# Kernel optimization log

Hardware: AMD Instinct MI355X
Metric: run time of the kernel (lower is better)

Reference implementation:

```python
import jax, jax.numpy as jnp
import numpy as np

B, C, L, K = 8, 128, 32768, 129  # batch, seq_len (channels), samples, filter length


def setup_inputs() -> dict:
    key = jax.random.key(0)
    k0, k1, k2, k3 = jax.random.split(key, 4)
    return {
        "x": jax.random.normal(k0, (B, C, L), dtype=jnp.float32),
        "weights_mag": jnp.ones((C, 1), dtype=jnp.float32),
        "weights_angle": jax.random.uniform(k1, (C, 1), dtype=jnp.float32),
        "kernel_real": jax.random.normal(k2, (K,), dtype=jnp.float32),
        "kernel_imag": jax.random.normal(k3, (K,), dtype=jnp.float32),
    }


def _matched_filter(x, kr, ki):
    # PyTorch F.conv1d is cross-correlation; mf_coeffs = conj(kernel) repeated per
    # channel (groups = C), so every channel is correlated with the SAME conj kernel.
    # Input is real (x.to(complex64) has zero imag), so:
    #   out = corr(x, conj(k)) = corr(x, kr) - 1j * corr(x, ki)
    b, c, l = x.shape
    kk = kr.shape[0]
    pad = kk // 2
    w = jnp.stack([kr, -ki])[:, None, :]  # [2, 1, K]: real and imag of conj kernel
    y = jax.lax.conv_general_dilated(
        x.reshape(b * c, 1, l), w,
        window_strides=(1,), padding=[(pad, pad)],
        dimension_numbers=("NCH", "OIH", "NCH"),
    )  # [B*C, 2, L]
    yr = y[:, 0].reshape(b, c, l)
    yi = y[:, 1].reshape(b, c, l)
    return yr + 1j * yi  # complex64


def reference(x, weights_mag, weights_angle, kernel_real, kernel_imag):
    batch = x.shape[0]
    y = _matched_filter(x, kernel_real, kernel_imag)          # [B, C, L] complex64
    phase = jnp.arctan(weights_angle)                          # [C, 1]
    norm_mag = batch * jax.nn.softmax(weights_mag, axis=0)     # [C, 1]
    scale = (norm_mag.astype(jnp.complex64) * jnp.exp(-1j * phase))  # [C, 1] complex
    return scale * y
```

## Files before the change

### kernel.cpp

```cpp
#include <hip/hip_runtime.h>
#include <hip/hip_bf16.h>
#include <math.h>

constexpr int Bc = 8, Cc = 128, Lc = 32768, Kc = 129, PAD = Kc / 2;

constexpr int ROWS   = 16;
constexpr int MLEN   = 1024;
constexpr int PSPAN  = MLEN + 144;
constexpr int PSTR   = 1176;
constexpr int THREADS= 256;
constexpr int NTILES = MLEN / 16;
constexpr int NWAVES = THREADS / 64;
constexpr int TPW    = NTILES / NWAVES;
constexpr int NQ     = PSPAN / 4;
constexpr int NF     = 19;

typedef __attribute__((ext_vector_type(8))) short short8;
typedef __attribute__((ext_vector_type(4))) float floatx4;

__device__ __forceinline__ unsigned short f2bf(float f) {
    return __builtin_bit_cast(unsigned short, __float2bfloat16(f));
}

__global__ void scale_kernel(const float* __restrict__ wm,
                             const float* __restrict__ wa,
                             float* __restrict__ ws, int C, float batchf) {
    int c = threadIdx.x;
    if (c >= C) return;
    float m = -1e30f;
    for (int i = 0; i < C; ++i) m = fmaxf(m, wm[i]);
    float s = 0.f;
    for (int i = 0; i < C; ++i) s += expf(wm[i] - m);
    float nm = batchf * expf(wm[c] - m) / s;
    float a = wa[c];
    float inv = rsqrtf(1.f + a * a);
    ws[2 * c]     = nm * inv;
    ws[2 * c + 1] = nm * a * inv;
}

__global__ __launch_bounds__(THREADS, 4)
void mf_kernel(const float* __restrict__ x,
               const float* __restrict__ kr,
               const float* __restrict__ ki,
               const float* __restrict__ sc_ss,
               float* __restrict__ out, int interleaved) {
    __shared__ __align__(16) unsigned short lx[ROWS * PSTR];

    const int bx   = blockIdx.x;
    const int bg   = blockIdx.y;
    const int row0 = bg * ROWS;
    const int P0   = bx * MLEN;
    const int s0   = P0 - PAD;

    const int tid  = threadIdx.x;
    const int lane = tid & 63;
    const int fh   = lane >> 4;
    const int fn   = lane & 15;
    const int wv   = tid >> 6;

    short8 ar[5], ai[5];
    #pragma unroll
    for (int d = 0; d < 5; ++d) {
        #pragma unroll
        for (int e = 0; e < 8; ++e) {
            int idx = 32 * d + 8 * fh + e - fn;
            bool ok = (idx >= 0) && (idx < Kc);
            ar[d][e] = (short)f2bf(ok ? kr[idx] : 0.f);
            ai[d][e] = (short)f2bf(ok ? ki[idx] : 0.f);
        }
    }

    const int srow = tid >> 4;
    const int scol = tid & 15;
    const float* __restrict__ xr = x + (size_t)(row0 + srow) * Lc;
    unsigned short* lrow = &lx[srow * PSTR];
    const bool interior = (s0 >= 0) && (s0 + PSPAN <= Lc);
    #pragma unroll
    for (int i = 0; i < NF; ++i) {
        const int i4 = scol + 16 * i;
        if (i4 < NQ) {
            const int g = s0 + 4 * i4;
            float4 v;
            if (interior) {
                v = *reinterpret_cast<const float4*>(xr + g);
            } else {
                v.x = (g + 0 >= 0 && g + 0 < Lc) ? xr[g + 0] : 0.f;
                v.y = (g + 1 >= 0 && g + 1 < Lc) ? xr[g + 1] : 0.f;
                v.z = (g + 2 >= 0 && g + 2 < Lc) ? xr[g + 2] : 0.f;
                v.w = (g + 3 >= 0 && g + 3 < Lc) ? xr[g + 3] : 0.f;
            }
            __hip_bfloat162 p0 = __float22bfloat162_rn(make_float2(v.x, v.y));
            __hip_bfloat162 p1 = __float22bfloat162_rn(make_float2(v.z, v.w));
            ushort2 u0, u1;
            __builtin_memcpy(&u0, &p0, 4);
            __builtin_memcpy(&u1, &p1, 4);
            ushort4 h;
            h.x = u0.x; h.y = u0.y; h.z = u1.x; h.w = u1.y;
            *reinterpret_cast<ushort4*>(&lrow[4 * i4]) = h;
        }
    }
    __syncthreads();

    const int ch = (row0 + fn) & (Cc - 1);
    const float scv = sc_ss[2 * ch];
    const float ssv = sc_ss[2 * ch + 1];

    #pragma unroll
    for (int jj = 0; jj < TPW; ++jj) {
        const int j  = wv * TPW + jj;
        const int pb = 16 * j;
        const unsigned short* lp = &lx[fn * PSTR + pb + 8 * fh];
        floatx4 cr = {0.f, 0.f, 0.f, 0.f};
        floatx4 cim = {0.f, 0.f, 0.f, 0.f};
        #pragma unroll
        for (int d = 0; d < 5; ++d) {
            short8 b = *reinterpret_cast<const short8*>(lp + 32 * d);
            cr  = __builtin_amdgcn_mfma_f32_16x16x32_bf16(ar[d], b, cr, 0, 0, 0);
            cim = __builtin_amdgcn_mfma_f32_16x16x32_bf16(ai[d], b, cim, 0, 0, 0);
        }
        const size_t obase = (size_t)(row0 + fn) * Lc + P0 + pb + 4 * fh;
        if (!interleaved) {
            float4 o;
            o.x = scv * cr[0] - ssv * cim[0];
            o.y = scv * cr[1] - ssv * cim[1];
            o.z = scv * cr[2] - ssv * cim[2];
            o.w = scv * cr[3] - ssv * cim[3];
            *reinterpret_cast<float4*>(out + obase) = o;
        } else {
            float2* o2 = reinterpret_cast<float2*>(out) + obase;
            #pragma unroll
            for (int r = 0; r < 4; ++r) {
                o2[r] = make_float2(scv * cr[r] - ssv * cim[r],
                                    -scv * cim[r] - ssv * cr[r]);
            }
        }
    }
}

extern "C" void kernel_launch(void* const* d_in, const int* in_sizes, int n_in,
                              void* d_out, int out_size, void* d_ws, size_t ws_size,
                              hipStream_t stream) {
    const float* x  = (const float*)d_in[0];
    const float* wm = (const float*)d_in[1];
    const float* wa = (const float*)d_in[2];
    const float* kr = (const float*)d_in[3];
    const float* ki = (const float*)d_in[4];
    float* out = (float*)d_out;
    float* ws  = (float*)d_ws;

    const int C = in_sizes[1];
    const long long N = (long long)Bc * Cc * Lc;
    const int interleaved = (out_size == 2 * N) ? 1 : 0;

    hipLaunchKernelGGL(scale_kernel, dim3(1), dim3(C), 0, stream,
                       wm, wa, ws, C, (float)Bc);

    dim3 grid(Lc / MLEN, (Bc * Cc) / ROWS);
    hipLaunchKernelGGL(mf_kernel, grid, dim3(THREADS), 0, stream,
                       x, kr, ki, ws, out, interleaved);
}
```

Before: 78.77 us.

## Batch global loads ahead of filter build and swizzle block order across L

Interior blocks now issue the first ten float4 global loads up front, build the bf16 filter fragments while those loads are in flight, then convert and store them and issue the remaining loads in a second batch. This is meant to hide global-load latency behind the kernel-fragment setup and keep more memory requests outstanding. The block x index is also permuted so consecutively scheduled blocks touch spread-out L segments, which may change cache and channel locality. The cost is higher register pressure from holding up to ten float4 values at once, which could hurt occupancy under the launch bound of four blocks.

New measurement: 112.7 us. 1.43x slower.

```diff
diff --git a/kernel.cpp b/kernel.cpp
--- a/kernel.cpp
+++ b/kernel.cpp
@@ -14,6 +14,8 @@
 constexpr int TPW    = NTILES / NWAVES;
 constexpr int NQ     = PSPAN / 4;
 constexpr int NF     = 19;
+constexpr int NB1    = 10;
+constexpr int NB2    = NF - NB1;
 
 typedef __attribute__((ext_vector_type(8))) short short8;
 typedef __attribute__((ext_vector_type(4))) float floatx4;
@@ -46,7 +48,7 @@
                float* __restrict__ out, int interleaved) {
     __shared__ __align__(16) unsigned short lx[ROWS * PSTR];
 
-    const int bx   = blockIdx.x;
+    const int bx   = ((blockIdx.x & 7) << 2) | (blockIdx.x >> 3);
     const int bg   = blockIdx.y;
     const int row0 = bg * ROWS;
     const int P0   = bx * MLEN;
@@ -58,45 +60,72 @@
     const int fn   = lane & 15;
     const int wv   = tid >> 6;
 
-    short8 ar[5], ai[5];
-    #pragma unroll
-    for (int d = 0; d < 5; ++d) {
-        #pragma unroll
-        for (int e = 0; e < 8; ++e) {
-            int idx = 32 * d + 8 * fh + e - fn;
-            bool ok = (idx >= 0) && (idx < Kc);
-            ar[d][e] = (short)f2bf(ok ? kr[idx] : 0.f);
-            ai[d][e] = (short)f2bf(ok ? ki[idx] : 0.f);
-        }
-    }
-
     const int srow = tid >> 4;
     const int scol = tid & 15;
     const float* __restrict__ xr = x + (size_t)(row0 + srow) * Lc;
     unsigned short* lrow = &lx[srow * PSTR];
     const bool interior = (s0 >= 0) && (s0 + PSPAN <= Lc);
-    #pragma unroll
-    for (int i = 0; i < NF; ++i) {
-        const int i4 = scol + 16 * i;
-        if (i4 < NQ) {
-            const int g = s0 + 4 * i4;
-            float4 v;
-            if (interior) {
-                v = *reinterpret_cast<const float4*>(xr + g);
-            } else {
+
+    short8 ar[5], ai[5];
+
+    auto BUILD_A = [&]() {
+        #pragma unroll
+        for (int d = 0; d < 5; ++d) {
+            #pragma unroll
+            for (int e = 0; e < 8; ++e) {
+                int idx = 32 * d + 8 * fh + e - fn;
+                bool ok = (idx >= 0) && (idx < Kc);
+                ar[d][e] = (short)f2bf(ok ? kr[idx] : 0.f);
+                ai[d][e] = (short)f2bf(ok ? ki[idx] : 0.f);
+            }
+        }
+    };
+
+    auto CVTW = [&](int i4, const float4& v) {
+        __hip_bfloat162 p0 = __float22bfloat162_rn(make_float2(v.x, v.y));
+        __hip_bfloat162 p1 = __float22bfloat162_rn(make_float2(v.z, v.w));
+        ushort2 u0, u1;
+        __builtin_memcpy(&u0, &p0, 4);
+        __builtin_memcpy(&u1, &p1, 4);
+        ushort4 h;
+        h.x = u0.x; h.y = u0.y; h.z = u1.x; h.w = u1.y;
+        *reinterpret_cast<ushort4*>(&lrow[4 * i4]) = h;
+    };
+
+    if (interior) {
+        float4 va[NB1];
+        #pragma unroll
+        for (int i = 0; i < NB1; ++i) {
+            va[i] = *reinterpret_cast<const float4*>(xr + s0 + 4 * (scol + 16 * i));
+        }
+        BUILD_A();
+        #pragma unroll
+        for (int i = 0; i < NB1; ++i) CVTW(scol + 16 * i, va[i]);
+        float4 vb[NB2];
+        #pragma unroll
+        for (int i = 0; i < NB2; ++i) {
+            const int i4 = scol + 16 * (NB1 + i);
+            if (i4 < NQ) vb[i] = *reinterpret_cast<const float4*>(xr + s0 + 4 * i4);
+        }
+        #pragma unroll
+        for (int i = 0; i < NB2; ++i) {
+            const int i4 = scol + 16 * (NB1 + i);
+            if (i4 < NQ) CVTW(i4, vb[i]);
+        }
+    } else {
+        BUILD_A();
+        #pragma unroll
+        for (int i = 0; i < NF; ++i) {
+            const int i4 = scol + 16 * i;
+            if (i4 < NQ) {
+                const int g = s0 + 4 * i4;
+                float4 v;
                 v.x = (g + 0 >= 0 && g + 0 < Lc) ? xr[g + 0] : 0.f;
                 v.y = (g + 1 >= 0 && g + 1 < Lc) ? xr[g + 1] : 0.f;
                 v.z = (g + 2 >= 0 && g + 2 < Lc) ? xr[g + 2] : 0.f;
                 v.w = (g + 3 >= 0 && g + 3 < Lc) ? xr[g + 3] : 0.f;
+                CVTW(i4, v);
             }
-            __hip_bfloat162 p0 = __float22bfloat162_rn(make_float2(v.x, v.y));
-            __hip_bfloat162 p1 = __float22bfloat162_rn(make_float2(v.z, v.w));
-            ushort2 u0, u1;
-            __builtin_memcpy(&u0, &p0, 4);
-            __builtin_memcpy(&u1, &p1, 4);
-            ushort4 h;
-            h.x = u0.x; h.y = u0.y; h.z = u1.x; h.w = u1.y;
-            *reinterpret_cast<ushort4*>(&lrow[4 * i4]) = h;
         }
     }
     __syncthreads();
```

## Load input directly from global into MFMA operands, dropping LDS staging

Applied to the files above, without the earlier changes.

Removes the shared-memory staging of the bf16 input tile and the block barrier. Each lane now reads its MFMA B operand straight from global memory per output tile and converts it to bf16 in registers. This saves LDS traffic and the sync, but each input element is now fetched several times across overlapping windows and relies on L1/L2 to absorb the reuse. Occupancy hint raised from 4 to 5 blocks per SM.

After: 199.8 us. 2.54x slower.

```diff
diff --git a/kernel.cpp b/kernel.cpp
--- a/kernel.cpp
+++ b/kernel.cpp
@@ -6,20 +6,32 @@
 
 constexpr int ROWS   = 16;
 constexpr int MLEN   = 1024;
-constexpr int PSPAN  = MLEN + 144;
-constexpr int PSTR   = 1176;
 constexpr int THREADS= 256;
-constexpr int NTILES = MLEN / 16;
-constexpr int NWAVES = THREADS / 64;
-constexpr int TPW    = NTILES / NWAVES;
-constexpr int NQ     = PSPAN / 4;
-constexpr int NF     = 19;
+constexpr int TPW    = 16;
 
 typedef __attribute__((ext_vector_type(8))) short short8;
 typedef __attribute__((ext_vector_type(4))) float floatx4;
 
 __device__ __forceinline__ unsigned short f2bf(float f) {
     return __builtin_bit_cast(unsigned short, __float2bfloat16(f));
+}
+
+__device__ __forceinline__ short8 cvt8(const float4& a, const float4& b) {
+    __hip_bfloat162 p0 = __float22bfloat162_rn(make_float2(a.x, a.y));
+    __hip_bfloat162 p1 = __float22bfloat162_rn(make_float2(a.z, a.w));
+    __hip_bfloat162 p2 = __float22bfloat162_rn(make_float2(b.x, b.y));
+    __hip_bfloat162 p3 = __float22bfloat162_rn(make_float2(b.z, b.w));
+    ushort2 u0, u1, u2, u3;
+    __builtin_memcpy(&u0, &p0, 4);
+    __builtin_memcpy(&u1, &p1, 4);
+    __builtin_memcpy(&u2, &p2, 4);
+    __builtin_memcpy(&u3, &p3, 4);
+    short8 r;
+    r[0] = (short)u0.x; r[1] = (short)u0.y;
+    r[2] = (short)u1.x; r[3] = (short)u1.y;
+    r[4] = (short)u2.x; r[5] = (short)u2.y;
+    r[6] = (short)u3.x; r[7] = (short)u3.y;
+    return r;
 }
 
 __global__ void scale_kernel(const float* __restrict__ wm,
@@ -38,19 +50,16 @@
     ws[2 * c + 1] = nm * a * inv;
 }
 
-__global__ __launch_bounds__(THREADS, 4)
+__global__ __launch_bounds__(THREADS, 5)
 void mf_kernel(const float* __restrict__ x,
                const float* __restrict__ kr,
                const float* __restrict__ ki,
                const float* __restrict__ sc_ss,
                float* __restrict__ out, int interleaved) {
-    __shared__ __align__(16) unsigned short lx[ROWS * PSTR];
-
     const int bx   = blockIdx.x;
     const int bg   = blockIdx.y;
     const int row0 = bg * ROWS;
     const int P0   = bx * MLEN;
-    const int s0   = P0 - PAD;
 
     const int tid  = threadIdx.x;
     const int lane = tid & 63;
@@ -70,55 +79,54 @@
         }
     }
 
-    const int srow = tid >> 4;
-    const int scol = tid & 15;
-    const float* __restrict__ xr = x + (size_t)(row0 + srow) * Lc;
-    unsigned short* lrow = &lx[srow * PSTR];
-    const bool interior = (s0 >= 0) && (s0 + PSPAN <= Lc);
-    #pragma unroll
-    for (int i = 0; i < NF; ++i) {
-        const int i4 = scol + 16 * i;
-        if (i4 < NQ) {
-            const int g = s0 + 4 * i4;
-            float4 v;
-            if (interior) {
-                v = *reinterpret_cast<const float4*>(xr + g);
-            } else {
-                v.x = (g + 0 >= 0 && g + 0 < Lc) ? xr[g + 0] : 0.f;
-                v.y = (g + 1 >= 0 && g + 1 < Lc) ? xr[g + 1] : 0.f;
-                v.z = (g + 2 >= 0 && g + 2 < Lc) ? xr[g + 2] : 0.f;
-                v.w = (g + 3 >= 0 && g + 3 < Lc) ? xr[g + 3] : 0.f;
-            }
-            __hip_bfloat162 p0 = __float22bfloat162_rn(make_float2(v.x, v.y));
-            __hip_bfloat162 p1 = __float22bfloat162_rn(make_float2(v.z, v.w));
-            ushort2 u0, u1;
-            __builtin_memcpy(&u0, &p0, 4);
-            __builtin_memcpy(&u1, &p1, 4);
-            ushort4 h;
-            h.x = u0.x; h.y = u0.y; h.z = u1.x; h.w = u1.y;
-            *reinterpret_cast<ushort4*>(&lrow[4 * i4]) = h;
-        }
-    }
-    __syncthreads();
-
     const int ch = (row0 + fn) & (Cc - 1);
     const float scv = sc_ss[2 * ch];
     const float ssv = sc_ss[2 * ch + 1];
 
+    const float* __restrict__ xrow = x + (size_t)(row0 + fn) * Lc;
+    const int j0 = (P0 >> 4) + wv * TPW;
+    const float* p = xrow + (16 * j0 - PAD + 8 * fh);
+
     #pragma unroll
-    for (int jj = 0; jj < TPW; ++jj) {
-        const int j  = wv * TPW + jj;
-        const int pb = 16 * j;
-        const unsigned short* lp = &lx[fn * PSTR + pb + 8 * fh];
-        floatx4 cr = {0.f, 0.f, 0.f, 0.f};
+    for (int jj = 0; jj < TPW; ++jj, p += 16) {
+        const int jt = j0 + jj;
+        const int sb = 16 * jt - PAD;
+        floatx4 cr  = {0.f, 0.f, 0.f, 0.f};
         floatx4 cim = {0.f, 0.f, 0.f, 0.f};
-        #pragma unroll
-        for (int d = 0; d < 5; ++d) {
-            short8 b = *reinterpret_cast<const short8*>(lp + 32 * d);
-            cr  = __builtin_amdgcn_mfma_f32_16x16x32_bf16(ar[d], b, cr, 0, 0, 0);
-            cim = __builtin_amdgcn_mfma_f32_16x16x32_bf16(ai[d], b, cim, 0, 0, 0);
+
+        if (sb >= 0 && sb + 160 <= Lc) {
+            float4 f[10];
+            #pragma unroll
+            for (int d = 0; d < 5; ++d) {
+                f[2 * d]     = *reinterpret_cast<const float4*>(p + 32 * d);
+                f[2 * d + 1] = *reinterpret_cast<const float4*>(p + 32 * d + 4);
+            }
+            #pragma unroll
+            for (int d = 0; d < 5; ++d) {
+                short8 b = cvt8(f[2 * d], f[2 * d + 1]);
+                cr  = __builtin_amdgcn_mfma_f32_16x16x32_bf16(ar[d], b, cr, 0, 0, 0);
+                cim = __builtin_amdgcn_mfma_f32_16x16x32_bf16(ai[d], b, cim, 0, 0, 0);
+            }
+        } else {
+            #pragma unroll
+            for (int d = 0; d < 5; ++d) {
+                float4 va, vb;
+                const int g0 = sb + 32 * d + 8 * fh;
+                va.x = (g0 + 0 >= 0 && g0 + 0 < Lc) ? xrow[g0 + 0] : 0.f;
+                va.y = (g0 + 1 >= 0 && g0 + 1 < Lc) ? xrow[g0 + 1] : 0.f;
+                va.z = (g0 + 2 >= 0 && g0 + 2 < Lc) ? xrow[g0 + 2] : 0.f;
+                va.w = (g0 + 3 >= 0 && g0 + 3 < Lc) ? xrow[g0 + 3] : 0.f;
+                vb.x = (g0 + 4 >= 0 && g0 + 4 < Lc) ? xrow[g0 + 4] : 0.f;
+                vb.y = (g0 + 5 >= 0 && g0 + 5 < Lc) ? xrow[g0 + 5] : 0.f;
+                vb.z = (g0 + 6 >= 0 && g0 + 6 < Lc) ? xrow[g0 + 6] : 0.f;
+                vb.w = (g0 + 7 >= 0 && g0 + 7 < Lc) ? xrow[g0 + 7] : 0.f;
+                short8 b = cvt8(va, vb);
+                cr  = __builtin_amdgcn_mfma_f32_16x16x32_bf16(ar[d], b, cr, 0, 0, 0);
+                cim = __builtin_amdgcn_mfma_f32_16x16x32_bf16(ai[d], b, cim, 0, 0, 0);
+            }
         }
-        const size_t obase = (size_t)(row0 + fn) * Lc + P0 + pb + 4 * fh;
+
+        const size_t obase = (size_t)(row0 + fn) * Lc + 16 * jt + 4 * fh;
         if (!interleaved) {
             float4 o;
             o.x = scv * cr[0] - ssv * cim[0];
```

## Pipeline input staging with async global-to-LDS loads over multiple chunks per block

Applied to the files above, without the earlier changes.

Each block now handles four consecutive 512-sample chunks with 512 threads. The next chunk's fp32 input is fetched straight into LDS with global_load_lds while MFMAs run on the current chunk, then converted to bf16 in a separate LDS buffer. The intent is to hide global load latency and spread the kernel-coefficient setup across more work. The cost is extra LDS traffic for the fp32 staging copy, more barriers per chunk, fewer blocks in the grid, and a halo of 256 samples loaded per 512 outputs rather than 144 per 1024.

New measurement: 77.66 us. No clear change (-1.4%).

```diff
diff --git a/kernel.cpp b/kernel.cpp
--- a/kernel.cpp
+++ b/kernel.cpp
@@ -5,21 +5,25 @@
 constexpr int Bc = 8, Cc = 128, Lc = 32768, Kc = 129, PAD = Kc / 2;
 
 constexpr int ROWS   = 16;
-constexpr int MLEN   = 1024;
-constexpr int PSPAN  = MLEN + 144;
-constexpr int PSTR   = 1176;
-constexpr int THREADS= 256;
-constexpr int NTILES = MLEN / 16;
-constexpr int NWAVES = THREADS / 64;
-constexpr int TPW    = NTILES / NWAVES;
-constexpr int NQ     = PSPAN / 4;
-constexpr int NF     = 19;
+constexpr int MLEN   = 512;
+constexpr int NCH    = 4;
+constexpr int STG    = 768;
+constexpr int F32STR = 772;
+constexpr int BF_STR = 776;
+constexpr int THREADS= 512;
+constexpr int TPW    = 4;
 
 typedef __attribute__((ext_vector_type(8))) short short8;
 typedef __attribute__((ext_vector_type(4))) float floatx4;
 
 __device__ __forceinline__ unsigned short f2bf(float f) {
     return __builtin_bit_cast(unsigned short, __float2bfloat16(f));
+}
+
+__device__ __forceinline__ void gload_lds16(const float* g, void* l) {
+    auto gp = (const __attribute__((address_space(1))) void*)g;
+    auto lp = (__attribute__((address_space(3))) void*)l;
+    __builtin_amdgcn_global_load_lds(gp, lp, 16, 0, 0);
 }
 
 __global__ void scale_kernel(const float* __restrict__ wm,
@@ -44,19 +48,18 @@
                const float* __restrict__ ki,
                const float* __restrict__ sc_ss,
                float* __restrict__ out, int interleaved) {
-    __shared__ __align__(16) unsigned short lx[ROWS * PSTR];
+    __shared__ __align__(16) float          lf[ROWS * F32STR];
+    __shared__ __align__(16) unsigned short lb[ROWS * BF_STR];
 
     const int bx   = blockIdx.x;
     const int bg   = blockIdx.y;
     const int row0 = bg * ROWS;
-    const int P0   = bx * MLEN;
-    const int s0   = P0 - PAD;
 
     const int tid  = threadIdx.x;
     const int lane = tid & 63;
+    const int wv   = tid >> 6;
     const int fh   = lane >> 4;
     const int fn   = lane & 15;
-    const int wv   = tid >> 6;
 
     short8 ar[5], ai[5];
     #pragma unroll
@@ -69,71 +72,116 @@
             ai[d][e] = (short)f2bf(ok ? ki[idx] : 0.f);
         }
     }
-
-    const int srow = tid >> 4;
-    const int scol = tid & 15;
-    const float* __restrict__ xr = x + (size_t)(row0 + srow) * Lc;
-    unsigned short* lrow = &lx[srow * PSTR];
-    const bool interior = (s0 >= 0) && (s0 + PSPAN <= Lc);
-    #pragma unroll
-    for (int i = 0; i < NF; ++i) {
-        const int i4 = scol + 16 * i;
-        if (i4 < NQ) {
-            const int g = s0 + 4 * i4;
-            float4 v;
-            if (interior) {
-                v = *reinterpret_cast<const float4*>(xr + g);
-            } else {
-                v.x = (g + 0 >= 0 && g + 0 < Lc) ? xr[g + 0] : 0.f;
-                v.y = (g + 1 >= 0 && g + 1 < Lc) ? xr[g + 1] : 0.f;
-                v.z = (g + 2 >= 0 && g + 2 < Lc) ? xr[g + 2] : 0.f;
-                v.w = (g + 3 >= 0 && g + 3 < Lc) ? xr[g + 3] : 0.f;
-            }
-            __hip_bfloat162 p0 = __float22bfloat162_rn(make_float2(v.x, v.y));
-            __hip_bfloat162 p1 = __float22bfloat162_rn(make_float2(v.z, v.w));
-            ushort2 u0, u1;
-            __builtin_memcpy(&u0, &p0, 4);
-            __builtin_memcpy(&u1, &p1, 4);
-            ushort4 h;
-            h.x = u0.x; h.y = u0.y; h.z = u1.x; h.w = u1.y;
-            *reinterpret_cast<ushort4*>(&lrow[4 * i4]) = h;
-        }
-    }
-    __syncthreads();
-
     const int ch = (row0 + fn) & (Cc - 1);
     const float scv = sc_ss[2 * ch];
     const float ssv = sc_ss[2 * ch + 1];
 
-    #pragma unroll
-    for (int jj = 0; jj < TPW; ++jj) {
-        const int j  = wv * TPW + jj;
-        const int pb = 16 * j;
-        const unsigned short* lp = &lx[fn * PSTR + pb + 8 * fh];
-        floatx4 cr = {0.f, 0.f, 0.f, 0.f};
-        floatx4 cim = {0.f, 0.f, 0.f, 0.f};
-        #pragma unroll
-        for (int d = 0; d < 5; ++d) {
-            short8 b = *reinterpret_cast<const short8*>(lp + 32 * d);
-            cr  = __builtin_amdgcn_mfma_f32_16x16x32_bf16(ar[d], b, cr, 0, 0, 0);
-            cim = __builtin_amdgcn_mfma_f32_16x16x32_bf16(ai[d], b, cim, 0, 0, 0);
-        }
-        const size_t obase = (size_t)(row0 + fn) * Lc + P0 + pb + 4 * fh;
-        if (!interleaved) {
-            float4 o;
-            o.x = scv * cr[0] - ssv * cim[0];
-            o.y = scv * cr[1] - ssv * cim[1];
-            o.z = scv * cr[2] - ssv * cim[2];
-            o.w = scv * cr[3] - ssv * cim[3];
-            *reinterpret_cast<float4*>(out + obase) = o;
+    auto s0_of = [&](int c) { return (bx * NCH + c) * MLEN - 2 * PAD + 64; };
+
+    auto is_edge = [&](int c) {
+        const int s0 = (bx * NCH + c) * MLEN - 64;
+        return (s0 < 0) || (s0 + STG > Lc);
+    };
+
+    auto DMA_STAGE = [&](int c) {
+        const int s0 = (bx * NCH + c) * MLEN - 64;
+        #pragma unroll
+        for (int rr = 0; rr < 2; ++rr) {
+            const int r = 2 * wv + rr;
+            const float* xr = x + (size_t)(row0 + r) * Lc + s0 + 4 * lane;
+            #pragma unroll
+            for (int p = 0; p < 3; ++p) {
+                gload_lds16(xr + 256 * p, (char*)lf + 3088 * r + 1024 * p);
+            }
+        }
+    };
+
+    auto EDGE_STAGE = [&](int c) {
+        const int s0 = (bx * NCH + c) * MLEN - 64;
+        const int r = tid >> 5;
+        const int scol = tid & 31;
+        const float* xr = x + (size_t)(row0 + r) * Lc;
+        #pragma unroll
+        for (int i = 0; i < 6; ++i) {
+            const int c4 = 4 * (scol + 32 * i);
+            const int g = s0 + c4;
+            float4 v;
+            v.x = (g + 0 >= 0 && g + 0 < Lc) ? xr[g + 0] : 0.f;
+            v.y = (g + 1 >= 0 && g + 1 < Lc) ? xr[g + 1] : 0.f;
+            v.z = (g + 2 >= 0 && g + 2 < Lc) ? xr[g + 2] : 0.f;
+            v.w = (g + 3 >= 0 && g + 3 < Lc) ? xr[g + 3] : 0.f;
+            *reinterpret_cast<float4*>(&lf[F32STR * r + c4]) = v;
+        }
+    };
+
+    auto CONV = [&]() {
+        #pragma unroll
+        for (int rr = 0; rr < 2; ++rr) {
+            const int r = 2 * wv + rr;
+            #pragma unroll
+            for (int p = 0; p < 3; ++p) {
+                const int dw = 256 * p + 4 * lane;
+                float4 v = *reinterpret_cast<const float4*>(&lf[F32STR * r + dw]);
+                __hip_bfloat162 p0 = __float22bfloat162_rn(make_float2(v.x, v.y));
+                __hip_bfloat162 p1 = __float22bfloat162_rn(make_float2(v.z, v.w));
+                ushort2 u0, u1;
+                __builtin_memcpy(&u0, &p0, 4);
+                __builtin_memcpy(&u1, &p1, 4);
+                ushort4 h; h.x = u0.x; h.y = u0.y; h.z = u1.x; h.w = u1.y;
+                *reinterpret_cast<ushort4*>(&lb[BF_STR * r + dw]) = h;
+            }
+        }
+    };
+
+    auto COMPUTE = [&](int c) {
+        const int P0 = (bx * NCH + c) * MLEN;
+        #pragma unroll
+        for (int jj = 0; jj < TPW; ++jj) {
+            const int j = wv * TPW + jj;
+            floatx4 cr = {0.f, 0.f, 0.f, 0.f};
+            floatx4 cim = {0.f, 0.f, 0.f, 0.f};
+            const unsigned short* lp = &lb[BF_STR * fn + 16 * j + 8 * fh];
+            #pragma unroll
+            for (int d = 0; d < 5; ++d) {
+                short8 b = *reinterpret_cast<const short8*>(lp + 32 * d);
+                cr  = __builtin_amdgcn_mfma_f32_16x16x32_bf16(ar[d], b, cr, 0, 0, 0);
+                cim = __builtin_amdgcn_mfma_f32_16x16x32_bf16(ai[d], b, cim, 0, 0, 0);
+            }
+            const size_t obase = (size_t)(row0 + fn) * Lc + P0 + 16 * j + 4 * fh;
+            if (!interleaved) {
+                float4 o;
+                o.x = scv * cr[0] - ssv * cim[0];
+                o.y = scv * cr[1] - ssv * cim[1];
+                o.z = scv * cr[2] - ssv * cim[2];
+                o.w = scv * cr[3] - ssv * cim[3];
+                *reinterpret_cast<float4*>(out + obase) = o;
+            } else {
+                float2* o2 = reinterpret_cast<float2*>(out) + obase;
+                #pragma unroll
+                for (int r = 0; r < 4; ++r) {
+                    o2[r] = make_float2(scv * cr[r] - ssv * cim[r],
+                                        -scv * cim[r] - ssv * cr[r]);
+                }
+            }
+        }
+    };
+
+    if (!is_edge(0)) DMA_STAGE(0);
+
+    #pragma unroll 1
+    for (int c = 0; c < NCH; ++c) {
+        if (is_edge(c)) {
+            EDGE_STAGE(c);
+            __syncthreads();
         } else {
-            float2* o2 = reinterpret_cast<float2*>(out) + obase;
-            #pragma unroll
-            for (int r = 0; r < 4; ++r) {
-                o2[r] = make_float2(scv * cr[r] - ssv * cim[r],
-                                    -scv * cim[r] - ssv * cr[r]);
-            }
-        }
+            asm volatile("s_waitcnt vmcnt(0)" ::: "memory");
+            __builtin_amdgcn_sched_barrier(0);
+        }
+        CONV();
+        __syncthreads();
+        if (c + 1 < NCH && !is_edge(c + 1)) DMA_STAGE(c + 1);
+        COMPUTE(c);
+        __syncthreads();
     }
 }
 
@@ -155,7 +203,7 @@
     hipLaunchKernelGGL(scale_kernel, dim3(1), dim3(C), 0, stream,
                        wm, wa, ws, C, (float)Bc);
 
-    dim3 grid(Lc / MLEN, (Bc * Cc) / ROWS);
+    dim3 grid(Lc / (MLEN * NCH), (Bc * Cc) / ROWS);
     hipLaunchKernelGGL(mf_kernel, grid, dim3(THREADS), 0, stream,
                        x, kr, ki, ws, out, interleaved);
 }
```
